# Kernel tuning notes

Hardware: AMD Instinct MI355X
Metric: run time of the kernel (lower is better)

The kernel has to match this reference:

```python
import jax, jax.numpy as jnp
import numpy as np

TAU = 32.0


def setup_inputs() -> dict:
    key = jax.random.key(0)
    k1, k2, k3, k4, k5 = jax.random.split(key, 5)
    B, IN, E, D, M = 32768, 768, 256, 9, 10
    feature = jax.random.normal(k1, (B, IN), dtype=jnp.float32)
    category = jax.random.randint(k2, (B,), 0, D)  # unused in forward math
    # nn.Linear(input_dim, emb_dim, bias=False) stores weight [emb_dim, input_dim]
    W_topic = jax.random.normal(k3, (E, IN), dtype=jnp.float32) * (1.0 / np.sqrt(IN))
    W_domain = jax.random.normal(k4, (E, IN), dtype=jnp.float32) * (1.0 / np.sqrt(IN))
    memory = jax.random.normal(k5, (D, M, E), dtype=jnp.float32)  # stacked domain memory banks
    return {"feature": feature, "category": category, "W_topic": W_topic,
            "W_domain": W_domain, "memory": memory}


def reference(feature, category, W_topic, W_domain, memory):
    # L2-normalize features along dim 1
    f = feature / jnp.linalg.norm(feature, axis=1, keepdims=True)
    topic = f @ W_topic.T      # [B, E]
    dom = f @ W_domain.T       # [B, E]
    # per-domain memory attention, batched over all D domains at once
    att = jax.nn.softmax(jnp.einsum('be,dme->bdm', topic, memory) * TAU, axis=-1)  # [B, D, M]
    sep = jnp.einsum('bdm,dme->bde', att, memory)                                   # [B, D, E]
    domain_att = jnp.einsum('bde,be->bd', sep, dom)                                 # [B, D]
    return jax.nn.softmax(domain_att * TAU, axis=1)[:, None, :]                     # [B, 1, D]
```

## Files before the change

kernel.cpp:

```cpp
#include <hip/hip_runtime.h>
#include <math.h>

typedef __attribute__((ext_vector_type(8))) short short8;
typedef __attribute__((ext_vector_type(4))) float f32x4;
typedef __attribute__((ext_vector_type(8))) unsigned short u16x8;

#define TAUF 32.0f

constexpr int B_LO_OFF = 12288;
constexpr int BUF_SZ   = 24576;
constexpr int CSTR     = 196;

__global__ __launch_bounds__(768) void precompute_pr(
    const float* __restrict__ Wt, const float* __restrict__ Wd,
    const float* __restrict__ mem, unsigned short* __restrict__ PRhi,
    unsigned short* __restrict__ PRlo) {
  int r0 = blockIdx.x * 6, t = threadIdx.x;
  if (r0 >= 180) {
    #pragma unroll
    for (int rr = 0; rr < 6; ++rr) {
      PRhi[(size_t)(r0 + rr) * 768 + t] = 0;
      PRlo[(size_t)(r0 + rr) * 768 + t] = 0;
    }
    return;
  }
  __shared__ float mlds[1536];
  const float* W = (r0 >= 90) ? Wd : Wt;
  int dm0 = (r0 >= 90) ? r0 - 90 : r0;
  for (int i = t; i < 1536; i += 768) mlds[i] = mem[(size_t)dm0 * 256 + i];
  __syncthreads();
  float a[6] = {0.f, 0.f, 0.f, 0.f, 0.f, 0.f};
  #pragma unroll 4
  for (int e = 0; e < 256; ++e) {
    float w = W[(size_t)e * 768 + t];
    #pragma unroll
    for (int rr = 0; rr < 6; ++rr) a[rr] += mlds[rr * 256 + e] * w;
  }
  #pragma unroll
  for (int rr = 0; rr < 6; ++rr) {
    unsigned int bu = __float_as_uint(a[rr]);
    unsigned short hi = (unsigned short)(bu >> 16);
    float hf = __uint_as_float(bu & 0xffff0000u);
    unsigned short lo = (unsigned short)(__float_as_uint(a[rr] - hf) >> 16);
    PRhi[(size_t)(r0 + rr) * 768 + t] = hi;
    PRlo[(size_t)(r0 + rr) * 768 + t] = lo;
  }
}

__global__ __launch_bounds__(256, 2) void fused_mfma(
    const float* __restrict__ feat, const unsigned short* __restrict__ PRhi,
    const unsigned short* __restrict__ PRlo, float* __restrict__ out) {
  __shared__ f32x4 smemv[3136];
  __shared__ float invn[64];
  __shared__ float sarr[576];
  char* smem = (char*)smemv;

  const int t    = threadIdx.x;
  const int lane = t & 63;
  const int wid  = t >> 6;
  const int rg   = wid >> 1;
  const int cg   = wid & 1;
  const int b0   = blockIdx.x * 64;

  const float* gA0 = feat + (size_t)(b0 + rg * 32 + (lane & 15)) * 768 +
                     ((lane >> 4) << 3);
  const float* gA1 = gA0 + 16 * 768;

  const int iid  = wid * 6;
  const int bc   = lane >> 2;
  const int bsw  = (lane & 3) ^ ((bc >> 1) & 3);
  const int bsrc = bc * 1536 + bsw * 16;

  const int bfr = ((lane & 15) << 6) |
                  ((((lane >> 4) ^ (((lane & 15) >> 1) & 3)) & 3) << 4);

  f32x4 acc0[6], acc1[6];
  #pragma unroll
  for (int j = 0; j < 6; ++j) {
    acc0[j] = (f32x4){0.f, 0.f, 0.f, 0.f};
    acc1[j] = (f32x4){0.f, 0.f, 0.f, 0.f};
  }
  float ssq0 = 0.f, ssq1 = 0.f;

  auto issueB = [&](int kt, int bb) {
    #pragma unroll
    for (int u = 0; u < 6; ++u) {
      int i  = iid + u;
      int pl = i >= 12;
      int ch = pl ? i - 12 : i;
      const unsigned short* basep = pl ? PRlo : PRhi;
      const char* gg = (const char*)basep + (size_t)ch * 16 * 1536 +
                       kt * 64 + bsrc;
      char* l = smem + bb * BUF_SZ + (pl ? B_LO_OFF : 0) + ch * 1024 +
                lane * 16;
      __builtin_amdgcn_global_load_lds((const unsigned int*)gg,
                                       (unsigned int*)l, 16, 0, 0);
    }
  };

  float4 Aa0, Aa1, Aa2, Aa3, Ab0, Ab1, Ab2, Ab3;
  auto loadAa = [&](int kt) {
    Aa0 = *(const float4*)(gA0 + kt * 32);
    Aa1 = *(const float4*)(gA0 + kt * 32 + 4);
    Aa2 = *(const float4*)(gA1 + kt * 32);
    Aa3 = *(const float4*)(gA1 + kt * 32 + 4);
  };
  auto loadAb = [&](int kt) {
    Ab0 = *(const float4*)(gA0 + kt * 32);
    Ab1 = *(const float4*)(gA0 + kt * 32 + 4);
    Ab2 = *(const float4*)(gA1 + kt * 32);
    Ab3 = *(const float4*)(gA1 + kt * 32 + 4);
  };

  short8 ah0, al0, ah1, al1;
  auto cvtCore = [&](float4 ra0a, float4 ra0b, float4 ra1a, float4 ra1b) {
    float x0[8] = {ra0a.x, ra0a.y, ra0a.z, ra0a.w, ra0b.x, ra0b.y, ra0b.z, ra0b.w};
    float x1[8] = {ra1a.x, ra1a.y, ra1a.z, ra1a.w, ra1b.x, ra1b.y, ra1b.z, ra1b.w};
    u16x8 h0, l0, h1, l1;
    #pragma unroll
    for (int e = 0; e < 8; ++e) {
      float x = x0[e];
      ssq0 += x * x;
      unsigned int bu = __float_as_uint(x);
      h0[e] = (unsigned short)(bu >> 16);
      l0[e] = (unsigned short)(__float_as_uint(x - __uint_as_float(bu & 0xffff0000u)) >> 16);
      float y = x1[e];
      ssq1 += y * y;
      unsigned int bv = __float_as_uint(y);
      h1[e] = (unsigned short)(bv >> 16);
      l1[e] = (unsigned short)(__float_as_uint(y - __uint_as_float(bv & 0xffff0000u)) >> 16);
    }
    ah0 = (short8)h0; al0 = (short8)l0; ah1 = (short8)h1; al1 = (short8)l1;
  };

  auto domfma = [&](int bb) {
    char* base = smem + bb * BUF_SZ;
    #pragma unroll
    for (int j = 0; j < 6; ++j) {
      int chb = (cg * 6 + j) * 1024;
      short8 bh = *(const short8*)(base + chb + bfr);
      short8 bl = *(const short8*)(base + B_LO_OFF + chb + bfr);
      acc0[j] = __builtin_amdgcn_mfma_f32_16x16x32_bf16(ah0, bh, acc0[j], 0, 0, 0);
      acc0[j] = __builtin_amdgcn_mfma_f32_16x16x32_bf16(al0, bh, acc0[j], 0, 0, 0);
      acc0[j] = __builtin_amdgcn_mfma_f32_16x16x32_bf16(ah0, bl, acc0[j], 0, 0, 0);
      acc1[j] = __builtin_amdgcn_mfma_f32_16x16x32_bf16(ah1, bh, acc1[j], 0, 0, 0);
      acc1[j] = __builtin_amdgcn_mfma_f32_16x16x32_bf16(al1, bh, acc1[j], 0, 0, 0);
      acc1[j] = __builtin_amdgcn_mfma_f32_16x16x32_bf16(ah1, bl, acc1[j], 0, 0, 0);
    }
  };

  issueB(0, 0);
  issueB(1, 1);
  loadAa(0);
  loadAb(1);
  asm volatile("s_waitcnt vmcnt(14)" ::: "memory");
  __builtin_amdgcn_sched_barrier(0);
  __builtin_amdgcn_s_barrier();

  for (int kp = 0; kp < 11; ++kp) {
    int kt = 2 * kp;
    cvtCore(Aa0, Aa1, Aa2, Aa3);
    domfma(0);
    __builtin_amdgcn_sched_barrier(0);
    __builtin_amdgcn_s_barrier();
    issueB(kt + 2, 0);
    loadAa(kt + 2);
    asm volatile("s_waitcnt vmcnt(14)" ::: "memory");
    __builtin_amdgcn_sched_barrier(0);
    __builtin_amdgcn_s_barrier();
    cvtCore(Ab0, Ab1, Ab2, Ab3);
    domfma(1);
    __builtin_amdgcn_sched_barrier(0);
    __builtin_amdgcn_s_barrier();
    issueB(kt + 3, 1);
    loadAb(kt + 3);
    asm volatile("s_waitcnt vmcnt(14)" ::: "memory");
    __builtin_amdgcn_sched_barrier(0);
    __builtin_amdgcn_s_barrier();
  }
  cvtCore(Aa0, Aa1, Aa2, Aa3);
  domfma(0);
  __builtin_amdgcn_sched_barrier(0);
  __builtin_amdgcn_s_barrier();
  asm volatile("s_waitcnt vmcnt(0)" ::: "memory");
  __builtin_amdgcn_sched_barrier(0);
  __builtin_amdgcn_s_barrier();
  cvtCore(Ab0, Ab1, Ab2, Ab3);
  domfma(1);

  float v0 = ssq0, v1 = ssq1;
  v0 += __shfl_xor(v0, 16, 64); v0 += __shfl_xor(v0, 32, 64);
  v1 += __shfl_xor(v1, 16, 64); v1 += __shfl_xor(v1, 32, 64);
  if (cg == 0 && lane < 16) {
    invn[rg * 32 + lane]      = rsqrtf(v0);
    invn[rg * 32 + 16 + lane] = rsqrtf(v1);
  }
  __syncthreads();

  float* Clds = (float*)smem;
  #pragma unroll
  for (int rt = 0; rt < 2; ++rt) {
    int rbase = rg * 32 + rt * 16 + ((lane >> 4) << 2);
    #pragma unroll
    for (int j = 0; j < 6; ++j) {
      int col = cg * 96 + j * 16 + (lane & 15);
      f32x4 v = rt ? acc1[j] : acc0[j];
      #pragma unroll
      for (int jj = 0; jj < 4; ++jj)
        Clds[(rbase + jj) * CSTR + col] = v[jj] * invn[rbase + jj];
    }
  }
  __syncthreads();

  for (int pid = t; pid < 576; pid += 256) {
    int row = pid / 9, d = pid - row * 9;
    const float* qp = Clds + row * CSTR + d * 10;
    const float* rp = qp + 90;
    float mx = qp[0];
    #pragma unroll
    for (int m = 1; m < 10; ++m) mx = fmaxf(mx, qp[m]);
    float s = 0.f, val = 0.f;
    #pragma unroll
    for (int m = 0; m < 10; ++m) {
      float e = __expf(TAUF * (qp[m] - mx));
      s += e;
      val += e * rp[m];
    }
    sarr[pid] = val / s;
  }
  __syncthreads();

  if (t < 64) {
    float v[9];
    #pragma unroll
    for (int d = 0; d < 9; ++d) v[d] = sarr[t * 9 + d];
    float mx = v[0];
    #pragma unroll
    for (int d = 1; d < 9; ++d) mx = fmaxf(mx, v[d]);
    float s = 0.f;
    float e[9];
    #pragma unroll
    for (int d = 0; d < 9; ++d) {
      e[d] = __expf(TAUF * (v[d] - mx));
      s += e[d];
    }
    float is = 1.f / s;
    #pragma unroll
    for (int d = 0; d < 9; ++d)
      out[(size_t)(b0 + t) * 9 + d] = e[d] * is;
  }
}

extern "C" void kernel_launch(void* const* d_in, const int* in_sizes, int n_in,
                              void* d_out, int out_size, void* d_ws, size_t ws_size,
                              hipStream_t stream) {
  const float* feat = (const float*)d_in[0];
  const float* Wt  = (const float*)d_in[2];
  const float* Wd  = (const float*)d_in[3];
  const float* mem = (const float*)d_in[4];
  float* outp = (float*)d_out;

  unsigned short* PRhi = (unsigned short*)d_ws;
  unsigned short* PRlo = PRhi + 192 * 768;

  precompute_pr<<<32, 768, 0, stream>>>(Wt, Wd, mem, PRhi, PRlo);
  const int B = in_sizes[1];
  fused_mfma<<<B / 64, 256, 0, stream>>>(feat, PRhi, PRlo, outp);
}
```

Before: 74.27 us.

## Load B fragments directly from global into registers instead of staging through LDS

```diff
diff --git a/kernel.cpp b/kernel.cpp
--- a/kernel.cpp
+++ b/kernel.cpp
@@ -7,9 +7,7 @@
 
 #define TAUF 32.0f
 
-constexpr int B_LO_OFF = 12288;
-constexpr int BUF_SZ   = 24576;
-constexpr int CSTR     = 196;
+constexpr int CSTR = 196;
 
 __global__ __launch_bounds__(768) void precompute_pr(
     const float* __restrict__ Wt, const float* __restrict__ Wd,
@@ -49,11 +47,10 @@
 
 __global__ __launch_bounds__(256, 2) void fused_mfma(
     const float* __restrict__ feat, const unsigned short* __restrict__ PRhi,
-    const unsigned short* __restrict__ PRlo, float* __restrict__ out) {
-  __shared__ f32x4 smemv[3136];
+    float* __restrict__ out) {
+  __shared__ float Clds[64 * CSTR];
   __shared__ float invn[64];
   __shared__ float sarr[576];
-  char* smem = (char*)smemv;
 
   const int t    = threadIdx.x;
   const int lane = t & 63;
@@ -66,13 +63,9 @@
                      ((lane >> 4) << 3);
   const float* gA1 = gA0 + 16 * 768;
 
-  const int iid  = wid * 6;
-  const int bc   = lane >> 2;
-  const int bsw  = (lane & 3) ^ ((bc >> 1) & 3);
-  const int bsrc = bc * 1536 + bsw * 16;
-
-  const int bfr = ((lane & 15) << 6) |
-                  ((((lane >> 4) ^ (((lane & 15) >> 1) & 3)) & 3) << 4);
+  constexpr size_t PLOFF = (size_t)192 * 768 * 2;
+  const char* gB = (const char*)PRhi +
+                   (size_t)(cg * 96 + (lane & 15)) * 1536 + ((lane >> 4) << 4);
 
   f32x4 acc0[6], acc1[6];
   #pragma unroll
@@ -82,23 +75,23 @@
   }
   float ssq0 = 0.f, ssq1 = 0.f;
 
-  auto issueB = [&](int kt, int bb) {
-    #pragma unroll
-    for (int u = 0; u < 6; ++u) {
-      int i  = iid + u;
-      int pl = i >= 12;
-      int ch = pl ? i - 12 : i;
-      const unsigned short* basep = pl ? PRlo : PRhi;
-      const char* gg = (const char*)basep + (size_t)ch * 16 * 1536 +
-                       kt * 64 + bsrc;
-      char* l = smem + bb * BUF_SZ + (pl ? B_LO_OFF : 0) + ch * 1024 +
-                lane * 16;
-      __builtin_amdgcn_global_load_lds((const unsigned int*)gg,
-                                       (unsigned int*)l, 16, 0, 0);
-    }
-  };
-
+  short8 Bah[6], Bal[6], Bbh[6], Bbl[6];
   float4 Aa0, Aa1, Aa2, Aa3, Ab0, Ab1, Ab2, Ab3;
+
+  auto loadBa = [&](int kt) {
+    #pragma unroll
+    for (int j = 0; j < 6; ++j) {
+      Bah[j] = *(const short8*)(gB + (size_t)j * 24576 + (size_t)kt * 64);
+      Bal[j] = *(const short8*)(gB + PLOFF + (size_t)j * 24576 + (size_t)kt * 64);
+    }
+  };
+  auto loadBb = [&](int kt) {
+    #pragma unroll
+    for (int j = 0; j < 6; ++j) {
+      Bbh[j] = *(const short8*)(gB + (size_t)j * 24576 + (size_t)kt * 64);
+      Bbl[j] = *(const short8*)(gB + PLOFF + (size_t)j * 24576 + (size_t)kt * 64);
+    }
+  };
   auto loadAa = [&](int kt) {
     Aa0 = *(const float4*)(gA0 + kt * 32);
     Aa1 = *(const float4*)(gA0 + kt * 32 + 4);
@@ -133,60 +126,49 @@
     ah0 = (short8)h0; al0 = (short8)l0; ah1 = (short8)h1; al1 = (short8)l1;
   };
 
-  auto domfma = [&](int bb) {
-    char* base = smem + bb * BUF_SZ;
-    #pragma unroll
-    for (int j = 0; j < 6; ++j) {
-      int chb = (cg * 6 + j) * 1024;
-      short8 bh = *(const short8*)(base + chb + bfr);
-      short8 bl = *(const short8*)(base + B_LO_OFF + chb + bfr);
-      acc0[j] = __builtin_amdgcn_mfma_f32_16x16x32_bf16(ah0, bh, acc0[j], 0, 0, 0);
-      acc0[j] = __builtin_amdgcn_mfma_f32_16x16x32_bf16(al0, bh, acc0[j], 0, 0, 0);
-      acc0[j] = __builtin_amdgcn_mfma_f32_16x16x32_bf16(ah0, bl, acc0[j], 0, 0, 0);
-      acc1[j] = __builtin_amdgcn_mfma_f32_16x16x32_bf16(ah1, bh, acc1[j], 0, 0, 0);
-      acc1[j] = __builtin_amdgcn_mfma_f32_16x16x32_bf16(al1, bh, acc1[j], 0, 0, 0);
-      acc1[j] = __builtin_amdgcn_mfma_f32_16x16x32_bf16(ah1, bl, acc1[j], 0, 0, 0);
-    }
-  };
-
-  issueB(0, 0);
-  issueB(1, 1);
+  auto mfmaA = [&]() {
+    #pragma unroll
+    for (int j = 0; j < 6; ++j) {
+      acc0[j] = __builtin_amdgcn_mfma_f32_16x16x32_bf16(ah0, Bah[j], acc0[j], 0, 0, 0);
+      acc0[j] = __builtin_amdgcn_mfma_f32_16x16x32_bf16(al0, Bah[j], acc0[j], 0, 0, 0);
+      acc0[j] = __builtin_amdgcn_mfma_f32_16x16x32_bf16(ah0, Bal[j], acc0[j], 0, 0, 0);
+      acc1[j] = __builtin_amdgcn_mfma_f32_16x16x32_bf16(ah1, Bah[j], acc1[j], 0, 0, 0);
+      acc1[j] = __builtin_amdgcn_mfma_f32_16x16x32_bf16(al1, Bah[j], acc1[j], 0, 0, 0);
+      acc1[j] = __builtin_amdgcn_mfma_f32_16x16x32_bf16(ah1, Bal[j], acc1[j], 0, 0, 0);
+    }
+  };
+  auto mfmaB = [&]() {
+    #pragma unroll
+    for (int j = 0; j < 6; ++j) {
+      acc0[j] = __builtin_amdgcn_mfma_f32_16x16x32_bf16(ah0, Bbh[j], acc0[j], 0, 0, 0);
+      acc0[j] = __builtin_amdgcn_mfma_f32_16x16x32_bf16(al0, Bbh[j], acc0[j], 0, 0, 0);
+      acc0[j] = __builtin_amdgcn_mfma_f32_16x16x32_bf16(ah0, Bbl[j], acc0[j], 0, 0, 0);
+      acc1[j] = __builtin_amdgcn_mfma_f32_16x16x32_bf16(ah1, Bbh[j], acc1[j], 0, 0, 0);
+      acc1[j] = __builtin_amdgcn_mfma_f32_16x16x32_bf16(al1, Bbh[j], acc1[j], 0, 0, 0);
+      acc1[j] = __builtin_amdgcn_mfma_f32_16x16x32_bf16(ah1, Bbl[j], acc1[j], 0, 0, 0);
+    }
+  };
+
+  loadBa(0);
   loadAa(0);
+  loadBb(1);
   loadAb(1);
-  asm volatile("s_waitcnt vmcnt(14)" ::: "memory");
-  __builtin_amdgcn_sched_barrier(0);
-  __builtin_amdgcn_s_barrier();
 
   for (int kp = 0; kp < 11; ++kp) {
     int kt = 2 * kp;
     cvtCore(Aa0, Aa1, Aa2, Aa3);
-    domfma(0);
-    __builtin_amdgcn_sched_barrier(0);
-    __builtin_amdgcn_s_barrier();
-    issueB(kt + 2, 0);
+    mfmaA();
+    loadBa(kt + 2);
     loadAa(kt + 2);
-    asm volatile("s_waitcnt vmcnt(14)" ::: "memory");
-    __builtin_amdgcn_sched_barrier(0);
-    __builtin_amdgcn_s_barrier();
     cvtCore(Ab0, Ab1, Ab2, Ab3);
-    domfma(1);
-    __builtin_amdgcn_sched_barrier(0);
-    __builtin_amdgcn_s_barrier();
-    issueB(kt + 3, 1);
+    mfmaB();
+    loadBb(kt + 3);
     loadAb(kt + 3);
-    asm volatile("s_waitcnt vmcnt(14)" ::: "memory");
-    __builtin_amdgcn_sched_barrier(0);
-    __builtin_amdgcn_s_barrier();
   }
   cvtCore(Aa0, Aa1, Aa2, Aa3);
-  domfma(0);
-  __builtin_amdgcn_sched_barrier(0);
-  __builtin_amdgcn_s_barrier();
-  asm volatile("s_waitcnt vmcnt(0)" ::: "memory");
-  __builtin_amdgcn_sched_barrier(0);
-  __builtin_amdgcn_s_barrier();
+  mfmaA();
   cvtCore(Ab0, Ab1, Ab2, Ab3);
-  domfma(1);
+  mfmaB();
 
   float v0 = ssq0, v1 = ssq1;
   v0 += __shfl_xor(v0, 16, 64); v0 += __shfl_xor(v0, 32, 64);
@@ -197,7 +179,6 @@
   }
   __syncthreads();
 
-  float* Clds = (float*)smem;
   #pragma unroll
   for (int rt = 0; rt < 2; ++rt) {
     int rbase = rg * 32 + rt * 16 + ((lane >> 4) << 2);
@@ -265,5 +246,5 @@
 
   precompute_pr<<<32, 768, 0, stream>>>(Wt, Wd, mem, PRhi, PRlo);
   const int B = in_sizes[1];
-  fused_mfma<<<B / 64, 256, 0, stream>>>(feat, PRhi, PRlo, outp);
+  fused_mfma<<<B / 64, 256, 0, stream>>>(feat, PRhi, outp);
 }
```

New measurement: 143.6 us. 1.93x slower.

## Double block to 128 rows with 8 waves sharing each staged B tile

Applied to the files above, without the earlier changes.

```diff
diff --git a/kernel.cpp b/kernel.cpp
--- a/kernel.cpp
+++ b/kernel.cpp
@@ -6,6 +6,8 @@
 typedef __attribute__((ext_vector_type(8))) unsigned short u16x8;
 
 #define TAUF 32.0f
+#define SB() __builtin_amdgcn_sched_barrier(0)
+#define BAR() __builtin_amdgcn_s_barrier()
 
 constexpr int B_LO_OFF = 12288;
 constexpr int BUF_SZ   = 24576;
@@ -47,11 +49,11 @@
   }
 }
 
-__global__ __launch_bounds__(256, 2) void fused_mfma(
+__global__ __launch_bounds__(512, 2) void fused_mfma(
     const float* __restrict__ feat, const unsigned short* __restrict__ PRhi,
     const unsigned short* __restrict__ PRlo, float* __restrict__ out) {
   __shared__ f32x4 smemv[3136];
-  __shared__ float invn[64];
+  __shared__ float invn[128];
   __shared__ float sarr[576];
   char* smem = (char*)smemv;
 
@@ -60,13 +62,13 @@
   const int wid  = t >> 6;
   const int rg   = wid >> 1;
   const int cg   = wid & 1;
-  const int b0   = blockIdx.x * 64;
+  const int b0   = blockIdx.x * 128;
 
   const float* gA0 = feat + (size_t)(b0 + rg * 32 + (lane & 15)) * 768 +
                      ((lane >> 4) << 3);
   const float* gA1 = gA0 + 16 * 768;
 
-  const int iid  = wid * 6;
+  const int iid  = wid * 3;
   const int bc   = lane >> 2;
   const int bsw  = (lane & 3) ^ ((bc >> 1) & 3);
   const int bsrc = bc * 1536 + bsw * 16;
@@ -84,7 +86,7 @@
 
   auto issueB = [&](int kt, int bb) {
     #pragma unroll
-    for (int u = 0; u < 6; ++u) {
+    for (int u = 0; u < 3; ++u) {
       int i  = iid + u;
       int pl = i >= 12;
       int ch = pl ? i - 12 : i;
@@ -114,8 +116,10 @@
 
   short8 ah0, al0, ah1, al1;
   auto cvtCore = [&](float4 ra0a, float4 ra0b, float4 ra1a, float4 ra1b) {
-    float x0[8] = {ra0a.x, ra0a.y, ra0a.z, ra0a.w, ra0b.x, ra0b.y, ra0b.z, ra0b.w};
-    float x1[8] = {ra1a.x, ra1a.y, ra1a.z, ra1a.w, ra1b.x, ra1b.y, ra1b.z, ra1b.w};
+    float x0[8] = {ra0a.x, ra0a.y, ra0a.z, ra0a.w,
+                   ra0b.x, ra0b.y, ra0b.z, ra0b.w};
+    float x1[8] = {ra1a.x, ra1a.y, ra1a.z, ra1a.w,
+                   ra1b.x, ra1b.y, ra1b.z, ra1b.w};
     u16x8 h0, l0, h1, l1;
     #pragma unroll
     for (int e = 0; e < 8; ++e) {
@@ -123,12 +127,14 @@
       ssq0 += x * x;
       unsigned int bu = __float_as_uint(x);
       h0[e] = (unsigned short)(bu >> 16);
-      l0[e] = (unsigned short)(__float_as_uint(x - __uint_as_float(bu & 0xffff0000u)) >> 16);
+      l0[e] = (unsigned short)(__float_as_uint(
+                  x - __uint_as_float(bu & 0xffff0000u)) >> 16);
       float y = x1[e];
       ssq1 += y * y;
       unsigned int bv = __float_as_uint(y);
       h1[e] = (unsigned short)(bv >> 16);
-      l1[e] = (unsigned short)(__float_as_uint(y - __uint_as_float(bv & 0xffff0000u)) >> 16);
+      l1[e] = (unsigned short)(__float_as_uint(
+                  y - __uint_as_float(bv & 0xffff0000u)) >> 16);
     }
     ah0 = (short8)h0; al0 = (short8)l0; ah1 = (short8)h1; al1 = (short8)l1;
   };
@@ -150,41 +156,34 @@
   };
 
   issueB(0, 0);
+  loadAa(0);
   issueB(1, 1);
-  loadAa(0);
   loadAb(1);
-  asm volatile("s_waitcnt vmcnt(14)" ::: "memory");
-  __builtin_amdgcn_sched_barrier(0);
-  __builtin_amdgcn_s_barrier();
+  asm volatile("s_waitcnt vmcnt(11)" ::: "memory");
+  SB(); BAR();
 
   for (int kp = 0; kp < 11; ++kp) {
     int kt = 2 * kp;
     cvtCore(Aa0, Aa1, Aa2, Aa3);
     domfma(0);
-    __builtin_amdgcn_sched_barrier(0);
-    __builtin_amdgcn_s_barrier();
+    SB(); BAR();
     issueB(kt + 2, 0);
     loadAa(kt + 2);
-    asm volatile("s_waitcnt vmcnt(14)" ::: "memory");
-    __builtin_amdgcn_sched_barrier(0);
-    __builtin_amdgcn_s_barrier();
+    asm volatile("s_waitcnt vmcnt(11)" ::: "memory");
+    SB(); BAR();
     cvtCore(Ab0, Ab1, Ab2, Ab3);
     domfma(1);
-    __builtin_amdgcn_sched_barrier(0);
-    __builtin_amdgcn_s_barrier();
+    SB(); BAR();
     issueB(kt + 3, 1);
     loadAb(kt + 3);
-    asm volatile("s_waitcnt vmcnt(14)" ::: "memory");
-    __builtin_amdgcn_sched_barrier(0);
-    __builtin_amdgcn_s_barrier();
+    asm volatile("s_waitcnt vmcnt(11)" ::: "memory");
+    SB(); BAR();
   }
   cvtCore(Aa0, Aa1, Aa2, Aa3);
   domfma(0);
-  __builtin_amdgcn_sched_barrier(0);
-  __builtin_amdgcn_s_barrier();
-  asm volatile("s_waitcnt vmcnt(0)" ::: "memory");
-  __builtin_amdgcn_sched_barrier(0);
-  __builtin_amdgcn_s_barrier();
+  SB(); BAR();
+  asm volatile("s_waitcnt vmcnt(4)" ::: "memory");
+  SB(); BAR();
   cvtCore(Ab0, Ab1, Ab2, Ab3);
   domfma(1);
 
@@ -198,56 +197,63 @@
   __syncthreads();
 
   float* Clds = (float*)smem;
-  #pragma unroll
-  for (int rt = 0; rt < 2; ++rt) {
-    int rbase = rg * 32 + rt * 16 + ((lane >> 4) << 2);
-    #pragma unroll
-    for (int j = 0; j < 6; ++j) {
-      int col = cg * 96 + j * 16 + (lane & 15);
-      f32x4 v = rt ? acc1[j] : acc0[j];
-      #pragma unroll
-      for (int jj = 0; jj < 4; ++jj)
-        Clds[(rbase + jj) * CSTR + col] = v[jj] * invn[rbase + jj];
-    }
-  }
-  __syncthreads();
-
-  for (int pid = t; pid < 576; pid += 256) {
-    int row = pid / 9, d = pid - row * 9;
-    const float* qp = Clds + row * CSTR + d * 10;
-    const float* rp = qp + 90;
-    float mx = qp[0];
-    #pragma unroll
-    for (int m = 1; m < 10; ++m) mx = fmaxf(mx, qp[m]);
-    float s = 0.f, val = 0.f;
-    #pragma unroll
-    for (int m = 0; m < 10; ++m) {
-      float e = __expf(TAUF * (qp[m] - mx));
-      s += e;
-      val += e * rp[m];
-    }
-    sarr[pid] = val / s;
-  }
-  __syncthreads();
-
-  if (t < 64) {
-    float v[9];
-    #pragma unroll
-    for (int d = 0; d < 9; ++d) v[d] = sarr[t * 9 + d];
-    float mx = v[0];
-    #pragma unroll
-    for (int d = 1; d < 9; ++d) mx = fmaxf(mx, v[d]);
-    float s = 0.f;
-    float e[9];
-    #pragma unroll
-    for (int d = 0; d < 9; ++d) {
-      e[d] = __expf(TAUF * (v[d] - mx));
-      s += e[d];
-    }
-    float is = 1.f / s;
-    #pragma unroll
-    for (int d = 0; d < 9; ++d)
-      out[(size_t)(b0 + t) * 9 + d] = e[d] * is;
+  for (int ph = 0; ph < 2; ++ph) {
+    if ((rg >> 1) == ph) {
+      int lrow = (rg & 1) * 32;
+      #pragma unroll
+      for (int rt = 0; rt < 2; ++rt) {
+        int rbase = lrow + rt * 16 + ((lane >> 4) << 2);
+        int grow  = ph * 64 + rbase;
+        #pragma unroll
+        for (int j = 0; j < 6; ++j) {
+          int col = cg * 96 + j * 16 + (lane & 15);
+          f32x4 v = rt ? acc1[j] : acc0[j];
+          #pragma unroll
+          for (int jj = 0; jj < 4; ++jj)
+            Clds[(rbase + jj) * CSTR + col] = v[jj] * invn[grow + jj];
+        }
+      }
+    }
+    __syncthreads();
+
+    for (int pid = t; pid < 576; pid += 512) {
+      int row = pid / 9, d = pid - row * 9;
+      const float* qp = Clds + row * CSTR + d * 10;
+      const float* rp = qp + 90;
+      float mx = qp[0];
+      #pragma unroll
+      for (int m = 1; m < 10; ++m) mx = fmaxf(mx, qp[m]);
+      float s = 0.f, val = 0.f;
+      #pragma unroll
+      for (int m = 0; m < 10; ++m) {
+        float e = __expf(TAUF * (qp[m] - mx));
+        s += e;
+        val += e * rp[m];
+      }
+      sarr[pid] = val / s;
+    }
+    __syncthreads();
+
+    if (t < 64) {
+      float v2[9];
+      #pragma unroll
+      for (int d = 0; d < 9; ++d) v2[d] = sarr[t * 9 + d];
+      float mx = v2[0];
+      #pragma unroll
+      for (int d = 1; d < 9; ++d) mx = fmaxf(mx, v2[d]);
+      float s = 0.f;
+      float e[9];
+      #pragma unroll
+      for (int d = 0; d < 9; ++d) {
+        e[d] = __expf(TAUF * (v2[d] - mx));
+        s += e[d];
+      }
+      float is = 1.f / s;
+      #pragma unroll
+      for (int d = 0; d < 9; ++d)
+        out[(size_t)(b0 + ph * 64 + t) * 9 + d] = e[d] * is;
+    }
+    __syncthreads();
   }
 }
 
@@ -265,5 +271,5 @@
 
   precompute_pr<<<32, 768, 0, stream>>>(Wt, Wd, mem, PRhi, PRlo);
   const int B = in_sizes[1];
-  fused_mfma<<<B / 64, 256, 0, stream>>>(feat, PRhi, PRlo, outp);
+  fused_mfma<<<B / 128, 512, 0, stream>>>(feat, PRhi, PRlo, outp);
 }
```

Measured after the change: 82.96 us. 1.12x slower.
